# Kernel tuning notes

Measured on AMD Instinct MI355X. Metric: run time of the kernel, lower is better.

The kernel has to match this reference:

```python
import jax, jax.numpy as jnp
import numpy as np

D = 768
H = 12
FF = 3072
B = 64
S = 197
NUM_ITERS = 5
DT = 0.1


def setup_inputs() -> dict:
    key = jax.random.key(0)
    ks = jax.random.split(key, 16)
    sc = 0.02
    inp = {
        'x': jax.random.normal(ks[0], (B, S, D), jnp.float32),
        # MultiheadAttention params (torch layout: in_proj_weight (3D, D))
        'in_proj_w': jax.random.normal(ks[1], (3 * D, D), jnp.float32) * sc,
        'in_proj_b': jnp.zeros((3 * D,), jnp.float32),
        'out_proj_w': jax.random.normal(ks[2], (D, D), jnp.float32) * sc,
        'out_proj_b': jnp.zeros((D,), jnp.float32),
        # LayerNorms
        'ln_attn_g': jnp.ones((D,), jnp.float32),
        'ln_attn_b': jnp.zeros((D,), jnp.float32),
        'ln1_g': jnp.ones((D,), jnp.float32),
        'ln1_b': jnp.zeros((D,), jnp.float32),
        'ln2_g': jnp.ones((D,), jnp.float32),
        'ln2_b': jnp.zeros((D,), jnp.float32),
        # INL dynamics MLP: Linear(D,D) -> GELU -> Linear(D,D)
        'inl_w1': jax.random.normal(ks[3], (D, D), jnp.float32) * sc,
        'inl_b1': jnp.zeros((D,), jnp.float32),
        'inl_w2': jax.random.normal(ks[4], (D, D), jnp.float32) * sc,
        'inl_b2': jnp.zeros((D,), jnp.float32),
        # FFN: Linear(D,FF) -> GELU -> Linear(FF,D)
        'ffn_w1': jax.random.normal(ks[5], (FF, D), jnp.float32) * sc,
        'ffn_b1': jnp.zeros((FF,), jnp.float32),
        'ffn_w2': jax.random.normal(ks[6], (D, FF), jnp.float32) * sc,
        'ffn_b2': jnp.zeros((D,), jnp.float32),
    }
    return inp


def _layernorm(x, g, b, eps=1e-5):
    mu = jnp.mean(x, axis=-1, keepdims=True)
    var = jnp.var(x, axis=-1, keepdims=True)
    return (x - mu) * jax.lax.rsqrt(var + eps) * g + b


def _mha(x, in_w, in_b, out_w, out_b):
    # x: (B,S,D); qkv projection per torch MultiheadAttention
    qkv = jnp.einsum('bsd,ed->bse', x, in_w) + in_b  # (B,S,3D)
    q, k, v = jnp.split(qkv, 3, axis=-1)
    dh = D // H
    q = q.reshape(q.shape[0], q.shape[1], H, dh)
    k = k.reshape(k.shape[0], k.shape[1], H, dh)
    v = v.reshape(v.shape[0], v.shape[1], H, dh)
    scores = jnp.einsum('bqhd,bkhd->bhqk', q, k) / jnp.sqrt(jnp.float32(dh))
    attn = jax.nn.softmax(scores, axis=-1)
    out = jnp.einsum('bhqk,bkhd->bqhd', attn, v)
    out = out.reshape(out.shape[0], out.shape[1], D)
    return jnp.einsum('bsd,ed->bse', out, out_w) + out_b


def _forward(x, in_proj_w, in_proj_b, out_proj_w, out_proj_b,
             ln_attn_g, ln_attn_b, ln1_g, ln1_b, ln2_g, ln2_b,
             inl_w1, inl_b1, inl_w2, inl_b2,
             ffn_w1, ffn_b1, ffn_w2, ffn_b2):
    xn = _layernorm(x, ln_attn_g, ln_attn_b)
    x = x + _mha(xn, in_proj_w, in_proj_b, out_proj_w, out_proj_b)

    # INL dynamics: 5-iter fixed-point loop on normalized state
    state = _layernorm(x, ln1_g, ln1_b)

    def step(state, _):
        h = jax.nn.gelu(jnp.einsum('bsd,ed->bse', state, inl_w1) + inl_b1,
                        approximate=False)
        delta = jnp.einsum('bse,de->bsd', h, inl_w2) + inl_b2
        return state + DT * delta, None

    state, _ = jax.lax.scan(step, state, None, length=NUM_ITERS)
    x = x + state

    # FFN
    xn2 = _layernorm(x, ln2_g, ln2_b)
    h = jax.nn.gelu(jnp.einsum('bsd,fd->bsf', xn2, ffn_w1) + ffn_b1,
                    approximate=False)
    x = x + jnp.einsum('bsf,df->bsd', h, ffn_w2) + ffn_b2
    return x


def reference(x, in_proj_w, in_proj_b, out_proj_w, out_proj_b,
              ln_attn_g, ln_attn_b, ln1_g, ln1_b, ln2_g, ln2_b,
              inl_w1, inl_b1, inl_w2, inl_b2,
              ffn_w1, ffn_b1, ffn_w2, ffn_b2):
    return _forward(x, in_proj_w, in_proj_b, out_proj_w, out_proj_b,
                    ln_attn_g, ln_attn_b, ln1_g, ln1_b, ln2_g, ln2_b,
                    inl_w1, inl_b1, inl_w2, inl_b2,
                    ffn_w1, ffn_b1, ffn_w2, ffn_b2)
```

## Files before the change

kernel.cpp:

```cpp
#include <hip/hip_runtime.h>
#include <hip/hip_bf16.h>
#include <cstdio>

typedef __bf16 bf16x4 __attribute__((ext_vector_type(4)));
typedef __bf16 bf16x8 __attribute__((ext_vector_type(8)));
typedef float  f32x4  __attribute__((ext_vector_type(4)));

#define NTOK 12608
#define DMODEL 768
#define SEQ 197

__device__ __forceinline__ float b2f(__bf16 v) { return (float)v; }

__device__ __forceinline__ float gelu_f(float x) {
    float y = 1.5957691216f * (x + 0.044715f * x * x * x);
    float e = __expf(y);
    float t = 1.f - 2.f / (e + 1.f);
    return 0.5f * x * (1.f + t);
}

__device__ __forceinline__ void gload16(const void* src, void* dst) {
    __builtin_amdgcn_global_load_lds(
        (const __attribute__((address_space(1))) void*)src,
        (__attribute__((address_space(3))) void*)dst,
        16, 0, 0);
}

struct CvtArgs {
    const float* src[6];
    __bf16* dst[6];
    int n4[6];
};
__global__ __launch_bounds__(256) void cvt_all_k(CvtArgs a)
{
#pragma unroll
    for (int t = 0; t < 6; ++t) {
        const float4* in = (const float4*)a.src[t];
        bf16x4* out = (bf16x4*)a.dst[t];
        const int n4 = a.n4[t];
        for (int i = blockIdx.x * 256 + threadIdx.x; i < n4; i += gridDim.x * 256) {
            float4 v = in[i];
            bf16x4 o;
            o[0] = (__bf16)v.x; o[1] = (__bf16)v.y; o[2] = (__bf16)v.z; o[3] = (__bf16)v.w;
            out[i] = o;
        }
    }
}

__global__ __launch_bounds__(256) void ln_k(const float* __restrict__ x,
                                            const float* __restrict__ g,
                                            const float* __restrict__ b,
                                            __bf16* __restrict__ out, int N)
{
    int wid = blockIdx.x * 4 + (threadIdx.x >> 6);
    if (wid >= N) return;
    int lane = threadIdx.x & 63;
    const float4* row = (const float4*)(x + (size_t)wid * DMODEL);
    float v[12];
    float s = 0.f, sq = 0.f;
#pragma unroll
    for (int j = 0; j < 3; ++j) {
        float4 u = row[lane + 64 * j];
        float f0 = u.x, f1 = u.y, f2 = u.z, f3 = u.w;
        v[j*4+0] = f0; v[j*4+1] = f1; v[j*4+2] = f2; v[j*4+3] = f3;
        s += f0 + f1 + f2 + f3;
        sq += f0*f0 + f1*f1 + f2*f2 + f3*f3;
    }
#pragma unroll
    for (int o = 32; o >= 1; o >>= 1) { s += __shfl_xor(s, o); sq += __shfl_xor(sq, o); }
    float mu = s * (1.f / DMODEL);
    float var = sq * (1.f / DMODEL) - mu * mu;
    float rstd = rsqrtf(var + 1e-5f);
    bf16x4* orow = (bf16x4*)(out + (size_t)wid * DMODEL);
    const float4* gg = (const float4*)g;
    const float4* bb = (const float4*)b;
#pragma unroll
    for (int j = 0; j < 3; ++j) {
        float4 gu = gg[lane + 64*j], bu = bb[lane + 64*j];
        bf16x4 o4;
        o4[0] = (__bf16)((v[j*4+0] - mu) * rstd * gu.x + bu.x);
        o4[1] = (__bf16)((v[j*4+1] - mu) * rstd * gu.y + bu.y);
        o4[2] = (__bf16)((v[j*4+2] - mu) * rstd * gu.z + bu.z);
        o4[3] = (__bf16)((v[j*4+3] - mu) * rstd * gu.w + bu.w);
        orow[lane + 64*j] = o4;
    }
}

__global__ __launch_bounds__(256) void addln_k(float* __restrict__ x1,
                                               const __bf16* __restrict__ st,
                                               const float* __restrict__ g,
                                               const float* __restrict__ b,
                                               __bf16* __restrict__ xn2, int N)
{
    int wid = blockIdx.x * 4 + (threadIdx.x >> 6);
    if (wid >= N) return;
    int lane = threadIdx.x & 63;
    float4* r1 = (float4*)(x1 + (size_t)wid * DMODEL);
    const bf16x4* r2 = (const bf16x4*)(st + (size_t)wid * DMODEL);
    float v[12];
    float s = 0.f, sq = 0.f;
#pragma unroll
    for (int j = 0; j < 3; ++j) {
        float4 u1 = r1[lane + 64*j];
        bf16x4 u2 = r2[lane + 64*j];
        float f0 = u1.x + b2f(u2[0]), f1 = u1.y + b2f(u2[1]);
        float f2 = u1.z + b2f(u2[2]), f3 = u1.w + b2f(u2[3]);
        v[j*4+0] = f0; v[j*4+1] = f1; v[j*4+2] = f2; v[j*4+3] = f3;
        s += f0 + f1 + f2 + f3;
        sq += f0*f0 + f1*f1 + f2*f2 + f3*f3;
        float4 o; o.x = f0; o.y = f1; o.z = f2; o.w = f3;
        r1[lane + 64*j] = o;
    }
#pragma unroll
    for (int o = 32; o >= 1; o >>= 1) { s += __shfl_xor(s, o); sq += __shfl_xor(sq, o); }
    float mu = s * (1.f / DMODEL);
    float var = sq * (1.f / DMODEL) - mu * mu;
    float rstd = rsqrtf(var + 1e-5f);
    bf16x4* on = (bf16x4*)(xn2 + (size_t)wid * DMODEL);
    const float4* gg = (const float4*)g;
    const float4* bb = (const float4*)b;
#pragma unroll
    for (int j = 0; j < 3; ++j) {
        float4 gu = gg[lane + 64*j], bu = bb[lane + 64*j];
        bf16x4 o4;
        o4[0] = (__bf16)((v[j*4+0] - mu) * rstd * gu.x + bu.x);
        o4[1] = (__bf16)((v[j*4+1] - mu) * rstd * gu.y + bu.y);
        o4[2] = (__bf16)((v[j*4+2] - mu) * rstd * gu.z + bu.z);
        o4[3] = (__bf16)((v[j*4+3] - mu) * rstd * gu.w + bu.w);
        on[lane + 64*j] = o4;
    }
}

template <int EPI>
__global__ __launch_bounds__(512) void gemm_k(const __bf16* __restrict__ A,
                                              const __bf16* __restrict__ W,
                                              const float* __restrict__ bias,
                                              const void* __restrict__ resv,
                                              void* __restrict__ outv,
                                              int Nv, int K)
{
    __shared__ __align__(16) __bf16 Al[2][128 * 64];
    __shared__ __align__(16) __bf16 Bl[2][128 * 64];
    const int tid = threadIdx.x;
    const int lane = tid & 63;
    const int wv = tid >> 6;
    const int wr = wv >> 2, wc = wv & 3;

    const int ncol = gridDim.x;
    const int nwg = ncol * gridDim.y;
    const int orig = blockIdx.x + ncol * blockIdx.y;
    const int q8 = nwg >> 3, r8 = nwg & 7;
    const int xcd = orig & 7, off8 = orig >> 3;
    const int wgid = (xcd < r8 ? xcd * (q8 + 1) : r8 * (q8 + 1) + (xcd - r8) * q8) + off8;
    const int bcol = (wgid % ncol) * 128;
    const int brow = (wgid / ncol) * 128;

    const int M = ncol * 128;
    const int srow = tid >> 3;
    const int scol = (tid & 7) * 8;
    const int sg = (((tid & 7) ^ (srow & 7)) << 3);
    const int lq = lane >> 4, lr = lane & 15;
    const int gsw = lr & 7;

    const __bf16* Arow[2];
    const __bf16* Wrow[2];
#pragma unroll
    for (int it = 0; it < 2; ++it) {
        int row = it * 64 + srow;
        int ar = brow + row; ar = ar < Nv ? ar : (Nv - 1);
        Arow[it] = A + (size_t)ar * K + sg;
        Wrow[it] = W + (size_t)(bcol + row) * K + sg;
    }

    f32x4 acc[4][2];
#pragma unroll
    for (int m = 0; m < 4; ++m)
#pragma unroll
        for (int n = 0; n < 2; ++n)
#pragma unroll
            for (int i = 0; i < 4; ++i) acc[m][n][i] = 0.f;

    const int nk = K >> 6;

#pragma unroll
    for (int it = 0; it < 2; ++it) {
        int row = it * 64 + srow;
        gload16(Arow[it], &Al[0][row * 64 + scol]);
        gload16(Wrow[it], &Bl[0][row * 64 + scol]);
    }
    __syncthreads();

    for (int t = 0; t < nk; ++t) {
        const int cur = t & 1;
        if (t + 1 < nk) {
            const int koff = (t + 1) << 6;
#pragma unroll
            for (int it = 0; it < 2; ++it) {
                int row = it * 64 + srow;
                gload16(Arow[it] + koff, &Al[cur ^ 1][row * 64 + scol]);
                gload16(Wrow[it] + koff, &Bl[cur ^ 1][row * 64 + scol]);
            }
        }
#pragma unroll
        for (int kk = 0; kk < 2; ++kk) {
            bf16x8 af[4], bfr[2];
            const int cg = ((kk * 4 + lq) ^ gsw) << 3;
#pragma unroll
            for (int m = 0; m < 4; ++m)
                af[m] = *(const bf16x8*)&Al[cur][(wr * 64 + m * 16 + lr) * 64 + cg];
#pragma unroll
            for (int n = 0; n < 2; ++n)
                bfr[n] = *(const bf16x8*)&Bl[cur][(wc * 32 + n * 16 + lr) * 64 + cg];
#pragma unroll
            for (int m = 0; m < 4; ++m)
#pragma unroll
                for (int n = 0; n < 2; ++n)
                    acc[m][n] = __builtin_amdgcn_mfma_f32_16x16x32_bf16(af[m], bfr[n], acc[m][n], 0, 0, 0);
        }
        __syncthreads();
    }

#pragma unroll
    for (int m = 0; m < 4; ++m) {
        int row0 = brow + wr * 64 + m * 16 + lq * 4;
#pragma unroll
        for (int n = 0; n < 2; ++n) {
            int col = bcol + wc * 32 + n * 16 + lr;
            float bv = bias[col];
#pragma unroll
            for (int i = 0; i < 4; ++i) {
                int row = row0 + i;
                if (row < Nv) {
                    float v = acc[m][n][i] + bv;
                    size_t off = (size_t)row * M + col;
                    if constexpr (EPI == 0) {
                        ((__bf16*)outv)[off] = (__bf16)v;
                    } else if constexpr (EPI == 1) {
                        ((float*)outv)[off] = v + ((const float*)resv)[off];
                    } else if constexpr (EPI == 2) {
                        ((__bf16*)outv)[off] = (__bf16)gelu_f(v);
                    } else {
                        ((__bf16*)outv)[off] = (__bf16)(b2f(((const __bf16*)resv)[off]) + 0.1f * v);
                    }
                }
            }
        }
    }
}

__global__ __launch_bounds__(256) void attn_k(const __bf16* __restrict__ qkv,
                                              __bf16* __restrict__ attn_out)
{
    constexpr int S = SEQ, LDP = 232, QKVW = 2304;
    __shared__ __align__(16) __bf16 Vt[64 * LDP];
    __shared__ __align__(16) __bf16 P[4][16 * LDP];
    const int bh = blockIdx.x;
    const int b = bh / 12, h = bh % 12;
    const size_t base = (size_t)b * S * QKVW;
    const int tid = threadIdx.x, lane = tid & 63, wv = tid >> 6;
    const int lq = lane >> 4, lr = lane & 15;

    for (int idx = tid; idx < 224 * 8; idx += 256) {
        int j = idx >> 3, d0 = (idx & 7) * 8;
        bf16x8 v8;
        if (j < S) v8 = *(const bf16x8*)(qkv + base + (size_t)j * QKVW + 1536 + h * 64 + d0);
        else {
#pragma unroll
            for (int e = 0; e < 8; ++e) v8[e] = (__bf16)0.f;
        }
#pragma unroll
        for (int e = 0; e < 8; ++e) Vt[(d0 + e) * LDP + j] = v8[e];
    }
    __syncthreads();

    for (int qt = wv; qt < 13; qt += 4) {
        int q0 = qt * 16;
        int qrow = q0 + lr; qrow = qrow < S ? qrow : (S - 1);
        bf16x8 aq[2];
#pragma unroll
        for (int kk = 0; kk < 2; ++kk)
            aq[kk] = *(const bf16x8*)(qkv + base + (size_t)qrow * QKVW + h * 64 + kk * 32 + lq * 8);

        f32x4 sc[14];
#pragma unroll
        for (int jf = 0; jf < 14; ++jf) {
#pragma unroll
            for (int i = 0; i < 4; ++i) sc[jf][i] = 0.f;
            int j = jf * 16 + lr; int jc = j < S ? j : (S - 1);
#pragma unroll
            for (int kk = 0; kk < 2; ++kk) {
                bf16x8 bk = *(const bf16x8*)(qkv + base + (size_t)jc * QKVW + 768 + h * 64 + kk * 32 + lq * 8);
                sc[jf] = __builtin_amdgcn_mfma_f32_16x16x32_bf16(aq[kk], bk, sc[jf], 0, 0, 0);
            }
        }
        bool colv[14];
#pragma unroll
        for (int jf = 0; jf < 14; ++jf) colv[jf] = (jf * 16 + lr) < S;
#pragma unroll
        for (int i = 0; i < 4; ++i) {
            float mx = -1.0e30f;
#pragma unroll
            for (int jf = 0; jf < 14; ++jf) {
                float sv = colv[jf] ? sc[jf][i] : -1.0e30f;
                sc[jf][i] = sv;
                mx = fmaxf(mx, sv);
            }
#pragma unroll
            for (int o = 8; o >= 1; o >>= 1) mx = fmaxf(mx, __shfl_xor(mx, o));
            float sm = 0.f;
#pragma unroll
            for (int jf = 0; jf < 14; ++jf) {
                float p = expf((sc[jf][i] - mx) * 0.125f);
                sc[jf][i] = p; sm += p;
            }
#pragma unroll
            for (int o = 8; o >= 1; o >>= 1) sm += __shfl_xor(sm, o);
            float inv = 1.f / sm;
#pragma unroll
            for (int jf = 0; jf < 14; ++jf)
                P[wv][(lq * 4 + i) * LDP + jf * 16 + lr] = (__bf16)(sc[jf][i] * inv);
        }
        f32x4 o4[4];
#pragma unroll
        for (int df = 0; df < 4; ++df)
#pragma unroll
            for (int i = 0; i < 4; ++i) o4[df][i] = 0.f;
#pragma unroll
        for (int ks = 0; ks < 7; ++ks) {
            bf16x8 pa = *(const bf16x8*)&P[wv][lr * LDP + ks * 32 + lq * 8];
#pragma unroll
            for (int df = 0; df < 4; ++df) {
                bf16x8 vb = *(const bf16x8*)&Vt[(df * 16 + lr) * LDP + ks * 32 + lq * 8];
                o4[df] = __builtin_amdgcn_mfma_f32_16x16x32_bf16(pa, vb, o4[df], 0, 0, 0);
            }
        }
#pragma unroll
        for (int df = 0; df < 4; ++df)
#pragma unroll
            for (int i = 0; i < 4; ++i) {
                int qr = q0 + lq * 4 + i;
                if (qr < S)
                    attn_out[((size_t)b * S + qr) * DMODEL + h * 64 + df * 16 + lr] = (__bf16)o4[df][i];
            }
    }
}

extern "C" void kernel_launch(void* const* d_in, const int* in_sizes, int n_in,
                              void* d_out, int out_size, void* d_ws, size_t ws_size,
                              hipStream_t stream) {
    const float* x      = (const float*)d_in[0];
    const float* in_w   = (const float*)d_in[1];
    const float* in_b   = (const float*)d_in[2];
    const float* out_w  = (const float*)d_in[3];
    const float* out_b  = (const float*)d_in[4];
    const float* lnA_g  = (const float*)d_in[5];
    const float* lnA_b  = (const float*)d_in[6];
    const float* ln1_g  = (const float*)d_in[7];
    const float* ln1_b  = (const float*)d_in[8];
    const float* ln2_g  = (const float*)d_in[9];
    const float* ln2_b  = (const float*)d_in[10];
    const float* inl_w1 = (const float*)d_in[11];
    const float* inl_b1 = (const float*)d_in[12];
    const float* inl_w2 = (const float*)d_in[13];
    const float* inl_b2 = (const float*)d_in[14];
    const float* ffn_w1 = (const float*)d_in[15];
    const float* ffn_b1 = (const float*)d_in[16];
    const float* ffn_w2 = (const float*)d_in[17];
    const float* ffn_b2 = (const float*)d_in[18];

    const int N = NTOK;
    const size_t sz_inw = (size_t)2304 * 768, sz_outw = (size_t)768 * 768;
    const size_t sz_i1 = (size_t)768 * 768, sz_i2 = (size_t)768 * 768;
    const size_t sz_f1 = (size_t)3072 * 768, sz_f2 = (size_t)768 * 3072;
    const size_t wtot = sz_inw + sz_outw + sz_i1 + sz_i2 + sz_f1 + sz_f2;

    const size_t bA = (size_t)N * 3072 * 2;
    const size_t bB = (size_t)N * 768 * 2;
    const size_t bS = (size_t)N * 768 * 2;
    const size_t bX = (size_t)N * 768 * 4;
    const size_t need = wtot * 2 + bA + bB + bS + bX;
    if (ws_size < need) {
        fprintf(stderr, "kernel_launch: ws_size %zu < required %zu\n", ws_size, need);
        return;
    }
    char* ws = (char*)d_ws;
    __bf16* w_in  = (__bf16*)ws;
    __bf16* w_out = w_in + sz_inw;
    __bf16* w_i1  = w_out + sz_outw;
    __bf16* w_i2  = w_i1 + sz_i1;
    __bf16* w_f1  = w_i2 + sz_i2;
    __bf16* w_f2  = w_f1 + sz_f1;
    char* p = ws + wtot * 2;
    __bf16* bufA = (__bf16*)p;            p += bA;
    __bf16* bufB = (__bf16*)p;            p += bB;
    __bf16* st   = (__bf16*)p;            p += bS;
    float*  x1   = (float*)p;

    dim3 blk(256), gblk(512);
    const int lnGrid = (N + 3) / 4;
    const int nrow = 99;

    CvtArgs ca;
    ca.src[0] = in_w;   ca.dst[0] = w_in;  ca.n4[0] = (int)(sz_inw / 4);
    ca.src[1] = out_w;  ca.dst[1] = w_out; ca.n4[1] = (int)(sz_outw / 4);
    ca.src[2] = inl_w1; ca.dst[2] = w_i1;  ca.n4[2] = (int)(sz_i1 / 4);
    ca.src[3] = inl_w2; ca.dst[3] = w_i2;  ca.n4[3] = (int)(sz_i2 / 4);
    ca.src[4] = ffn_w1; ca.dst[4] = w_f1;  ca.n4[4] = (int)(sz_f1 / 4);
    ca.src[5] = ffn_w2; ca.dst[5] = w_f2;  ca.n4[5] = (int)(sz_f2 / 4);
    cvt_all_k<<<dim3(1024), blk, 0, stream>>>(ca);

    ln_k<<<dim3(lnGrid), blk, 0, stream>>>(x, lnA_g, lnA_b, bufB, N);
    gemm_k<0><<<dim3(18, nrow), gblk, 0, stream>>>(bufB, w_in, in_b, nullptr, bufA, N, 768);
    attn_k<<<dim3(768), blk, 0, stream>>>(bufA, bufB);
    gemm_k<1><<<dim3(6, nrow), gblk, 0, stream>>>(bufB, w_out, out_b, x, x1, N, 768);
    ln_k<<<dim3(lnGrid), blk, 0, stream>>>(x1, ln1_g, ln1_b, st, N);
    for (int it = 0; it < 5; ++it) {
        gemm_k<2><<<dim3(6, nrow), gblk, 0, stream>>>(st, w_i1, inl_b1, nullptr, bufA, N, 768);
        gemm_k<3><<<dim3(6, nrow), gblk, 0, stream>>>(bufA, w_i2, inl_b2, st, st, N, 768);
    }
    addln_k<<<dim3(lnGrid), blk, 0, stream>>>(x1, st, ln2_g, ln2_b, bufB, N);
    gemm_k<2><<<dim3(24, nrow), gblk, 0, stream>>>(bufB, w_f1, ffn_b1, nullptr, bufA, N, 768);
    gemm_k<1><<<dim3(6, nrow), gblk, 0, stream>>>(bufA, w_f2, ffn_b2, x1, (float*)d_out, N, 3072);
}
```

Measured before the change: 829.4 us.

## Add 256x128 tile GEMM for wide projections and split attention query tiles

Adds a second GEMM kernel with 256-row by 128-column tiles and a 4x4 MFMA accumulator per wave, used for the QKV projection and the FFN up-projection. This reuses each weight tile across more rows and cuts the number of workgroups. Attention is also split into two blocks per batch-head, each handling half the query tiles, to double parallelism. The cost is that each attention block now reloads the whole V transpose and K, and the larger GEMM tile needs more LDS and registers, which can lower occupancy.

```diff
diff --git a/kernel.cpp b/kernel.cpp
--- a/kernel.cpp
+++ b/kernel.cpp
@@ -181,7 +181,6 @@
             for (int i = 0; i < 4; ++i) acc[m][n][i] = 0.f;
 
     const int nk = K >> 6;
-
 #pragma unroll
     for (int it = 0; it < 2; ++it) {
         int row = it * 64 + srow;
@@ -248,13 +247,134 @@
     }
 }
 
+template <int EPI>
+__global__ __launch_bounds__(512) void gemm2_k(const __bf16* __restrict__ A,
+                                               const __bf16* __restrict__ W,
+                                               const float* __restrict__ bias,
+                                               const void* __restrict__ resv,
+                                               void* __restrict__ outv,
+                                               int Nv, int K)
+{
+    __shared__ __align__(16) __bf16 Al[2][256 * 64];
+    __shared__ __align__(16) __bf16 Bl[2][128 * 64];
+    const int tid = threadIdx.x;
+    const int lane = tid & 63;
+    const int wv = tid >> 6;
+    const int wr = wv >> 1, wc = wv & 1;
+
+    const int ncol = gridDim.x;
+    const int nwg = ncol * gridDim.y;
+    const int orig = blockIdx.x + ncol * blockIdx.y;
+    const int q8 = nwg >> 3, r8 = nwg & 7;
+    const int xcd = orig & 7, off8 = orig >> 3;
+    const int wgid = (xcd < r8 ? xcd * (q8 + 1) : r8 * (q8 + 1) + (xcd - r8) * q8) + off8;
+    const int bcol = (wgid % ncol) * 128;
+    const int brow = (wgid / ncol) * 256;
+
+    const int M = ncol * 128;
+    const int srow = tid >> 3;
+    const int scol = (tid & 7) * 8;
+    const int sg = (((tid & 7) ^ (srow & 7)) << 3);
+    const int lq = lane >> 4, lr = lane & 15;
+    const int gsw = lr & 7;
+
+    const __bf16* Arow[4];
+    const __bf16* Wrow[2];
+#pragma unroll
+    for (int it = 0; it < 4; ++it) {
+        int row = it * 64 + srow;
+        int ar = brow + row; ar = ar < Nv ? ar : (Nv - 1);
+        Arow[it] = A + (size_t)ar * K + sg;
+    }
+#pragma unroll
+    for (int it = 0; it < 2; ++it) {
+        int row = it * 64 + srow;
+        Wrow[it] = W + (size_t)(bcol + row) * K + sg;
+    }
+
+    f32x4 acc[4][4];
+#pragma unroll
+    for (int m = 0; m < 4; ++m)
+#pragma unroll
+        for (int n = 0; n < 4; ++n)
+#pragma unroll
+            for (int i = 0; i < 4; ++i) acc[m][n][i] = 0.f;
+
+    const int nk = K >> 6;
+#pragma unroll
+    for (int it = 0; it < 4; ++it)
+        gload16(Arow[it], &Al[0][(it * 64 + srow) * 64 + scol]);
+#pragma unroll
+    for (int it = 0; it < 2; ++it)
+        gload16(Wrow[it], &Bl[0][(it * 64 + srow) * 64 + scol]);
+    __syncthreads();
+
+    for (int t = 0; t < nk; ++t) {
+        const int cur = t & 1;
+        if (t + 1 < nk) {
+            const int koff = (t + 1) << 6;
+#pragma unroll
+            for (int it = 0; it < 4; ++it)
+                gload16(Arow[it] + koff, &Al[cur ^ 1][(it * 64 + srow) * 64 + scol]);
+#pragma unroll
+            for (int it = 0; it < 2; ++it)
+                gload16(Wrow[it] + koff, &Bl[cur ^ 1][(it * 64 + srow) * 64 + scol]);
+        }
+#pragma unroll
+        for (int kk = 0; kk < 2; ++kk) {
+            bf16x8 af[4], bfr[4];
+            const int cg = ((kk * 4 + lq) ^ gsw) << 3;
+#pragma unroll
+            for (int m = 0; m < 4; ++m)
+                af[m] = *(const bf16x8*)&Al[cur][(wr * 64 + m * 16 + lr) * 64 + cg];
+#pragma unroll
+            for (int n = 0; n < 4; ++n)
+                bfr[n] = *(const bf16x8*)&Bl[cur][(wc * 64 + n * 16 + lr) * 64 + cg];
+#pragma unroll
+            for (int m = 0; m < 4; ++m)
+#pragma unroll
+                for (int n = 0; n < 4; ++n)
+                    acc[m][n] = __builtin_amdgcn_mfma_f32_16x16x32_bf16(af[m], bfr[n], acc[m][n], 0, 0, 0);
+        }
+        __syncthreads();
+    }
+
+#pragma unroll
+    for (int m = 0; m < 4; ++m) {
+        int row0 = brow + wr * 64 + m * 16 + lq * 4;
+#pragma unroll
+        for (int n = 0; n < 4; ++n) {
+            int col = bcol + wc * 64 + n * 16 + lr;
+            float bv = bias[col];
+#pragma unroll
+            for (int i = 0; i < 4; ++i) {
+                int row = row0 + i;
+                if (row < Nv) {
+                    float v = acc[m][n][i] + bv;
+                    size_t off = (size_t)row * M + col;
+                    if constexpr (EPI == 0) {
+                        ((__bf16*)outv)[off] = (__bf16)v;
+                    } else if constexpr (EPI == 1) {
+                        ((float*)outv)[off] = v + ((const float*)resv)[off];
+                    } else if constexpr (EPI == 2) {
+                        ((__bf16*)outv)[off] = (__bf16)gelu_f(v);
+                    } else {
+                        ((__bf16*)outv)[off] = (__bf16)(b2f(((const __bf16*)resv)[off]) + 0.1f * v);
+                    }
+                }
+            }
+        }
+    }
+}
+
 __global__ __launch_bounds__(256) void attn_k(const __bf16* __restrict__ qkv,
                                               __bf16* __restrict__ attn_out)
 {
     constexpr int S = SEQ, LDP = 232, QKVW = 2304;
     __shared__ __align__(16) __bf16 Vt[64 * LDP];
     __shared__ __align__(16) __bf16 P[4][16 * LDP];
-    const int bh = blockIdx.x;
+    const int bh = blockIdx.x >> 1;
+    const int half = blockIdx.x & 1;
     const int b = bh / 12, h = bh % 12;
     const size_t base = (size_t)b * S * QKVW;
     const int tid = threadIdx.x, lane = tid & 63, wv = tid >> 6;
@@ -273,7 +393,7 @@
     }
     __syncthreads();
 
-    for (int qt = wv; qt < 13; qt += 4) {
+    for (int qt = wv + half * 4; qt < 13; qt += 8) {
         int q0 = qt * 16;
         int qrow = q0 + lr; qrow = qrow < S ? qrow : (S - 1);
         bf16x8 aq[2];
@@ -399,6 +519,7 @@
     dim3 blk(256), gblk(512);
     const int lnGrid = (N + 3) / 4;
     const int nrow = 99;
+    const int nrow2 = 50;
 
     CvtArgs ca;
     ca.src[0] = in_w;   ca.dst[0] = w_in;  ca.n4[0] = (int)(sz_inw / 4);
@@ -410,8 +531,8 @@
     cvt_all_k<<<dim3(1024), blk, 0, stream>>>(ca);
 
     ln_k<<<dim3(lnGrid), blk, 0, stream>>>(x, lnA_g, lnA_b, bufB, N);
-    gemm_k<0><<<dim3(18, nrow), gblk, 0, stream>>>(bufB, w_in, in_b, nullptr, bufA, N, 768);
-    attn_k<<<dim3(768), blk, 0, stream>>>(bufA, bufB);
+    gemm2_k<0><<<dim3(18, nrow2), gblk, 0, stream>>>(bufB, w_in, in_b, nullptr, bufA, N, 768);
+    attn_k<<<dim3(1536), blk, 0, stream>>>(bufA, bufB);
     gemm_k<1><<<dim3(6, nrow), gblk, 0, stream>>>(bufB, w_out, out_b, x, x1, N, 768);
     ln_k<<<dim3(lnGrid), blk, 0, stream>>>(x1, ln1_g, ln1_b, st, N);
     for (int it = 0; it < 5; ++it) {
@@ -419,6 +540,6 @@
         gemm_k<3><<<dim3(6, nrow), gblk, 0, stream>>>(bufA, w_i2, inl_b2, st, st, N, 768);
     }
     addln_k<<<dim3(lnGrid), blk, 0, stream>>>(x1, st, ln2_g, ln2_b, bufB, N);
-    gemm_k<2><<<dim3(24, nrow), gblk, 0, stream>>>(bufB, w_f1, ffn_b1, nullptr, bufA, N, 768);
+    gemm2_k<2><<<dim3(24, nrow2), gblk, 0, stream>>>(bufB, w_f1, ffn_b1, nullptr, bufA, N, 768);
     gemm_k<1><<<dim3(6, nrow), gblk, 0, stream>>>(bufA, w_f2, ffn_b2, x1, (float*)d_out, N, 3072);
 }
```

Result: slower. 866.0 us (+4.4%).
